# Optimization experiments

Hardware: AMD Instinct MI355X
Metric: run time of the kernel (lower is better)

Reference implementation:

```python
import jax, jax.numpy as jnp
import numpy as np


def _attention(q, k, v, causal):
    # q,k,v: (B, S, H, D) -> matches flash_attn_func input layout
    B, Sq, H, D = q.shape
    Sk = k.shape[1]
    scale = 1.0 / jnp.sqrt(jnp.asarray(D, dtype=q.dtype))
    # scores: (B, H, Sq, Sk)
    scores = jnp.einsum('bqhd,bkhd->bhqk', q, k) * scale
    if causal:
        # position i attends to j <= i (standard causal mask, Sq == Sk here)
        mask = jnp.tril(jnp.ones((Sq, Sk), dtype=bool))
        scores = jnp.where(mask[None, None], scores, jnp.asarray(-jnp.inf, dtype=scores.dtype))
    probs = jax.nn.softmax(scores, axis=-1)
    out = jnp.einsum('bhqk,bkhd->bqhd', probs, v)
    return out


def setup_inputs() -> dict:
    key = jax.random.key(0)
    kq, kk, kv = jax.random.split(key, 3)
    B, S, H, D = 2, 2048, 16, 128
    q = jax.random.normal(kq, (B, S, H, D), dtype=jnp.float32)
    k = jax.random.normal(kk, (B, S, H, D), dtype=jnp.float32)
    v = jax.random.normal(kv, (B, S, H, D), dtype=jnp.float32)
    return {"q": q, "k": k, "v": v, "causal": 1}


def reference(q, k, v, causal):
    return _attention(q, k, v, bool(causal))
```

## Files before the change

kernel.cpp:

```cpp
#include <hip/hip_runtime.h>

typedef short bf16x8 __attribute__((ext_vector_type(8)));
typedef float f32x16 __attribute__((ext_vector_type(16)));

constexpr int S = 2048;
constexpr int H = 16;
constexpr int D = 128;
constexpr int BM = 128;
constexpr int TILE = 8192;
constexpr int KSTR = 136;
constexpr int MST  = 33;


__device__ inline unsigned int pk2(float a, float b) {
    unsigned int ua = __builtin_bit_cast(unsigned int, a);
    unsigned int ub = __builtin_bit_cast(unsigned int, b);
    ua += 0x7fffu + ((ua >> 16) & 1u);
    ub += 0x7fffu + ((ub >> 16) & 1u);
    return (ua >> 16) | (ub & 0xffff0000u);
}

__global__ __launch_bounds__(256) void cvt_kv(const float* __restrict__ K,
                                              const float* __restrict__ V,
                                              unsigned short* __restrict__ Kb,
                                              unsigned short* __restrict__ Vtb) {
    __shared__ unsigned short Kst[64 * KSTR];
    __shared__ unsigned short Vst[64 * KSTR];
    __shared__ unsigned short Vout[TILE];
    const int tid = threadIdx.x;
    const int t   = blockIdx.x;
    const int bh  = blockIdx.y;
    const int b = bh >> 4, h = bh & 15;
    const size_t base = ((size_t)(b * S + t * 64) * H + h) * D;

    #pragma unroll
    for (int u = 0; u < 4; ++u) {
        const int c   = tid + 256 * u;
        const int n   = c >> 4;
        const int off = (c & 15) * 8;
        const float* pk = K + base + (size_t)n * (H * D) + off;
        float4 f0 = *(const float4*)pk;
        float4 f1 = *(const float4*)(pk + 4);
        unsigned int w[4];
        w[0] = pk2(f0.x, f0.y); w[1] = pk2(f0.z, f0.w);
        w[2] = pk2(f1.x, f1.y); w[3] = pk2(f1.z, f1.w);
        *(uint4*)&Kst[n * KSTR + off] = *(const uint4*)w;
        const float* pv = V + base + (size_t)n * (H * D) + off;
        f0 = *(const float4*)pv;
        f1 = *(const float4*)(pv + 4);
        w[0] = pk2(f0.x, f0.y); w[1] = pk2(f0.z, f0.w);
        w[2] = pk2(f1.x, f1.y); w[3] = pk2(f1.z, f1.w);
        *(uint4*)&Vst[n * KSTR + off] = *(const uint4*)w;
    }
    __syncthreads();

    unsigned short* outK = Kb + ((size_t)bh * 32 + t) * TILE;
    #pragma unroll
    for (int u = 0; u < 4; ++u) {
        const int s = u * 256 + tid;
        const int chunk = s >> 6;
        const int row   = s & 63;
        *(uint4*)(outK + s * 8) = *(const uint4*)&Kst[row * KSTR + chunk * 8];
    }

    const int d  = tid >> 1;
    const int kh = (tid & 1) * 32;
    unsigned short tmp[32];
    #pragma unroll
    for (int m = 0; m < 32; ++m) {
        const int sig = kh + m;
        const int k = (sig & ~12) | ((sig & 4) << 1) | ((sig & 8) >> 1);
        tmp[m] = Vst[k * KSTR + d];
    }
    #pragma unroll
    for (int uu = 0; uu < 4; ++uu) {
        const int cc = (kh >> 3) + uu;
        *(uint4*)&Vout[(cc * 128 + d) * 8] = *(const uint4*)&tmp[uu * 8];
    }
    __syncthreads();
    unsigned short* outV = Vtb + ((size_t)bh * 32 + t) * TILE;
    #pragma unroll
    for (int u = 0; u < 4; ++u) {
        const int s = u * 256 + tid;
        *(uint4*)(outV + s * 8) = *(const uint4*)&Vout[s * 8];
    }
}

__global__ __launch_bounds__(512, 2) void fa_fwd(
    const float* __restrict__ Q,
    const unsigned short* __restrict__ Kb,
    const unsigned short* __restrict__ Vtb,
    const int* __restrict__ causal_p,
    float* __restrict__ Op)
{
    __shared__ float mbf[4][64 * MST];
    __shared__ float lbf[4][32];

    const int tid  = threadIdx.x;
    const int w    = tid >> 6;
    const int lane = tid & 63;
    const int ln   = lane & 31;
    const int half = lane >> 5;
    const int qw   = w & 3;
    const int nt   = w >> 2;

    int bh, qp;
    if (gridDim.x == 8 && gridDim.y == 32) {
        const int lid = blockIdx.x + (blockIdx.y << 3);
        const int xcd = lid & 7;
        const int ii  = lid >> 3;
        bh = (xcd << 2) + (ii & 3);
        qp = ii >> 2;
    } else {
        bh = blockIdx.y;
        qp = blockIdx.x;
    }
    const int b = bh >> 4;
    const int h = bh & 15;
    const int causal = *causal_p;
    const float cfold = 0.12751743f;

    const unsigned short* Kc = Kb  + (size_t)bh * (32 * TILE);
    const unsigned short* Vc = Vtb + (size_t)bh * (32 * TILE);
    const int koff  = half * 512 + nt * 256 + ln * 8;
    const int vkoff = (nt * 4 + half) * 1024 + ln * 8;

    #pragma unroll 1
    for (int ph = 0; ph < 2; ++ph) {
        const int qblk  = ph ? (15 - qp) : qp;
        const int q0    = qblk * BM;
        const int qrow0 = q0 + qw * 32;
        const int jmax  = causal ? ((q0 + BM - 1) >> 6) : (S / 64 - 1);

        bf16x8 qf[8];
        {
            const size_t rowoff = ((size_t)(b * S + qrow0 + ln) * H + h) * D;
            #pragma unroll
            for (int c = 0; c < 8; ++c) {
                float4 f0 = *(const float4*)(Q + rowoff + c * 16 + half * 8);
                float4 f1 = *(const float4*)(Q + rowoff + c * 16 + half * 8 + 4);
                unsigned int t[4];
                t[0] = pk2(f0.x * cfold, f0.y * cfold);
                t[1] = pk2(f0.z * cfold, f0.w * cfold);
                t[2] = pk2(f1.x * cfold, f1.y * cfold);
                t[3] = pk2(f1.z * cfold, f1.w * cfold);
                qf[c] = *(const bf16x8*)t;
            }
        }

        f32x16 o[4];
        #pragma unroll
        for (int dt = 0; dt < 4; ++dt)
            #pragma unroll
            for (int r = 0; r < 16; ++r) o[dt][r] = 0.0f;
        float l0 = 0.0f, l1 = 0.0f;

        uint4 kr[8], vr[8];
        if ((!causal) || (nt * 32 <= qrow0 + 31)) {
            #pragma unroll
            for (int c = 0; c < 8; ++c)
                kr[c] = *(const uint4*)(Kc + c * 1024 + koff);
            #pragma unroll
            for (int i = 0; i < 8; ++i)
                vr[i] = *(const uint4*)(Vc + (i >> 2) * 2048 + (i & 3) * 256 + vkoff);
        }

        #pragma unroll 1
        for (int j = 0; j <= jmax; ++j) {
            const bool aj = (!causal) || (j * 64 + nt * 32 <= qrow0 + 31);
            const bool an = (j < jmax) &&
                            ((!causal) || ((j + 1) * 64 + nt * 32 <= qrow0 + 31));

            f32x16 sacc;
            if (aj) {
                #pragma unroll
                for (int r = 0; r < 16; ++r) sacc[r] = 0.0f;
                __builtin_amdgcn_s_setprio(1);
                #pragma unroll
                for (int c = 0; c < 8; ++c) {
                    bf16x8 kf = *(const bf16x8*)&kr[c];
                    sacc = __builtin_amdgcn_mfma_f32_32x32x16_bf16(kf, qf[c], sacc, 0, 0, 0);
                }
                __builtin_amdgcn_s_setprio(0);
            }
            if (an) {
                const unsigned short* kt = Kc + (size_t)(j + 1) * TILE;
                #pragma unroll
                for (int c = 0; c < 8; ++c)
                    kr[c] = *(const uint4*)(kt + c * 1024 + koff);
            }

            if (aj) {
                const int thr  = qrow0 + ln - j * 64;
                const bool full = (!causal) || (j * 64 + 63 <= qrow0);
                __builtin_amdgcn_s_setprio(1);
                #pragma unroll
                for (int win2 = 0; win2 < 2; ++win2) {
                    unsigned int pw[4];
                    #pragma unroll
                    for (int d2 = 0; d2 < 4; ++d2) {
                        const int r0 = win2 * 8 + 2 * d2;
                        const int r1 = r0 + 1;
                        float e0 = __builtin_amdgcn_exp2f(sacc[r0]);
                        float e1 = __builtin_amdgcn_exp2f(sacc[r1]);
                        if (!full) {
                            const int k0 = nt * 32 + (r0 & 3) + 8 * (r0 >> 2) + 4 * half;
                            const int k1 = nt * 32 + (r1 & 3) + 8 * (r1 >> 2) + 4 * half;
                            if (k0 > thr) e0 = 0.0f;
                            if (k1 > thr) e1 = 0.0f;
                        }
                        l0 += e0; l1 += e1;
                        pw[d2] = pk2(e0, e1);
                    }
                    bf16x8 pf = *(const bf16x8*)pw;
                    #pragma unroll
                    for (int dt = 0; dt < 4; ++dt) {
                        bf16x8 vf = *(const bf16x8*)&vr[win2 * 4 + dt];
                        o[dt] = __builtin_amdgcn_mfma_f32_32x32x16_bf16(vf, pf, o[dt], 0, 0, 0);
                    }
                }
                __builtin_amdgcn_s_setprio(0);
            }
            if (an) {
                const unsigned short* vt = Vc + (size_t)(j + 1) * TILE;
                #pragma unroll
                for (int i = 0; i < 8; ++i)
                    vr[i] = *(const uint4*)(vt + (i >> 2) * 2048 + (i & 3) * 256 + vkoff);
            }
        }

        const float l = l0 + l1;
        const float lp = l + __shfl_xor(l, 32);
        float* mb = mbf[qw];
        if (w >= 4) {
            #pragma unroll
            for (int dt = 0; dt < 2; ++dt)
                #pragma unroll
                for (int r = 0; r < 16; ++r)
                    mb[lane * MST + dt * 16 + r] = o[dt][r];
            if (half == 0) lbf[qw][ln] = lp;
        }
        __syncthreads();
        float ltot = 1.0f;
        if (w < 4) {
            #pragma unroll
            for (int dt = 0; dt < 2; ++dt)
                #pragma unroll
                for (int r = 0; r < 16; ++r)
                    o[dt][r] += mb[lane * MST + dt * 16 + r];
            ltot = lp + lbf[qw][ln];
        }
        __syncthreads();
        if (w >= 4) {
            #pragma unroll
            for (int dt = 2; dt < 4; ++dt)
                #pragma unroll
                for (int r = 0; r < 16; ++r)
                    mb[lane * MST + (dt - 2) * 16 + r] = o[dt][r];
        }
        __syncthreads();
        if (w < 4) {
            #pragma unroll
            for (int dt = 2; dt < 4; ++dt)
                #pragma unroll
                for (int r = 0; r < 16; ++r)
                    o[dt][r] += mb[lane * MST + (dt - 2) * 16 + r];

            const float inv = 1.0f / ltot;
            float* op = Op + ((size_t)(b * S + qrow0 + ln) * H + h) * D;
            #pragma unroll
            for (int dt = 0; dt < 4; ++dt)
                #pragma unroll
                for (int rq = 0; rq < 4; ++rq) {
                    float4 st;
                    st.x = o[dt][rq * 4 + 0] * inv;
                    st.y = o[dt][rq * 4 + 1] * inv;
                    st.z = o[dt][rq * 4 + 2] * inv;
                    st.w = o[dt][rq * 4 + 3] * inv;
                    *(float4*)(op + dt * 32 + 8 * rq + 4 * half) = st;
                }
        }
        __syncthreads();
    }
}

extern "C" void kernel_launch(void* const* d_in, const int* in_sizes, int n_in,
                              void* d_out, int out_size, void* d_ws, size_t ws_size,
                              hipStream_t stream) {
    const int B = in_sizes[0] / (S * H * D);
    unsigned short* Kb  = (unsigned short*)d_ws;
    unsigned short* Vtb = Kb + (size_t)B * S * H * D;

    cvt_kv<<<dim3(S / 64, B * H), 256, 0, stream>>>(
        (const float*)d_in[1], (const float*)d_in[2], Kb, Vtb);
    fa_fwd<<<dim3(8, B * H), 512, 0, stream>>>(
        (const float*)d_in[0], Kb, Vtb, (const int*)d_in[3], (float*)d_out);
}
```

Baseline: 187.2 us.

## Split KV tiles across two wave groups with 1024-thread blocks

Doubles the block to 16 waves, so each query block's KV tiles are split between two wave groups that take alternating 64-key tiles. The partial O and row sums from the three extra groups are merged through enlarged shared buffers before the final normalisation. This shortens each wave's serial KV loop and raises the waves in flight per block. In exchange it allows only one block per CU, uses more shared memory, and adds a heavier reduction step.

New measurement: 738.4 us. 295% more time.

```diff
diff --git a/kernel.cpp b/kernel.cpp
--- a/kernel.cpp
+++ b/kernel.cpp
@@ -86,15 +86,15 @@
     }
 }
 
-__global__ __launch_bounds__(512, 2) void fa_fwd(
+__global__ __launch_bounds__(1024, 1) void fa_fwd(
     const float* __restrict__ Q,
     const unsigned short* __restrict__ Kb,
     const unsigned short* __restrict__ Vtb,
     const int* __restrict__ causal_p,
     float* __restrict__ Op)
 {
-    __shared__ float mbf[4][64 * MST];
-    __shared__ float lbf[4][32];
+    __shared__ float mbf[3][4][64 * MST];
+    __shared__ float lbf[3][4][32];
 
     const int tid  = threadIdx.x;
     const int w    = tid >> 6;
@@ -102,7 +102,9 @@
     const int ln   = lane & 31;
     const int half = lane >> 5;
     const int qw   = w & 3;
-    const int nt   = w >> 2;
+    const int nt   = (w >> 2) & 1;
+    const int jt   = w >> 3;
+    const int pi   = w >> 2;
 
     int bh, qp;
     if (gridDim.x == 8 && gridDim.y == 32) {
@@ -130,7 +132,8 @@
         const int qblk  = ph ? (15 - qp) : qp;
         const int q0    = qblk * BM;
         const int qrow0 = q0 + qw * 32;
-        const int jmax  = causal ? ((q0 + BM - 1) >> 6) : (S / 64 - 1);
+        const int T     = causal ? (2 * qblk + 2) : (S / 64);
+        const int I     = T >> 1;
 
         bf16x8 qf[8];
         {
@@ -156,20 +159,23 @@
         float l0 = 0.0f, l1 = 0.0f;
 
         uint4 kr[8], vr[8];
-        if ((!causal) || (nt * 32 <= qrow0 + 31)) {
+        if ((!causal) || (jt * 64 + nt * 32 <= qrow0 + 31)) {
+            const unsigned short* kt = Kc + (size_t)jt * TILE;
+            const unsigned short* vt = Vc + (size_t)jt * TILE;
             #pragma unroll
             for (int c = 0; c < 8; ++c)
-                kr[c] = *(const uint4*)(Kc + c * 1024 + koff);
+                kr[c] = *(const uint4*)(kt + c * 1024 + koff);
             #pragma unroll
             for (int i = 0; i < 8; ++i)
-                vr[i] = *(const uint4*)(Vc + (i >> 2) * 2048 + (i & 3) * 256 + vkoff);
+                vr[i] = *(const uint4*)(vt + (i >> 2) * 2048 + (i & 3) * 256 + vkoff);
         }
 
         #pragma unroll 1
-        for (int j = 0; j <= jmax; ++j) {
-            const bool aj = (!causal) || (j * 64 + nt * 32 <= qrow0 + 31);
-            const bool an = (j < jmax) &&
-                            ((!causal) || ((j + 1) * 64 + nt * 32 <= qrow0 + 31));
+        for (int i = 0; i < I; ++i) {
+            const int jj = 2 * i + jt;
+            const bool aj = (!causal) || (jj * 64 + nt * 32 <= qrow0 + 31);
+            const bool an = (i + 1 < I) &&
+                            ((!causal) || ((jj + 2) * 64 + nt * 32 <= qrow0 + 31));
 
             f32x16 sacc;
             if (aj) {
@@ -184,15 +190,15 @@
                 __builtin_amdgcn_s_setprio(0);
             }
             if (an) {
-                const unsigned short* kt = Kc + (size_t)(j + 1) * TILE;
+                const unsigned short* kt = Kc + (size_t)(jj + 2) * TILE;
                 #pragma unroll
                 for (int c = 0; c < 8; ++c)
                     kr[c] = *(const uint4*)(kt + c * 1024 + koff);
             }
 
             if (aj) {
-                const int thr  = qrow0 + ln - j * 64;
-                const bool full = (!causal) || (j * 64 + 63 <= qrow0);
+                const int thr  = qrow0 + ln - jj * 64;
+                const bool full = (!causal) || (jj * 64 + 63 <= qrow0);
                 __builtin_amdgcn_s_setprio(1);
                 #pragma unroll
                 for (int win2 = 0; win2 < 2; ++win2) {
@@ -222,36 +228,42 @@
                 __builtin_amdgcn_s_setprio(0);
             }
             if (an) {
-                const unsigned short* vt = Vc + (size_t)(j + 1) * TILE;
-                #pragma unroll
-                for (int i = 0; i < 8; ++i)
-                    vr[i] = *(const uint4*)(vt + (i >> 2) * 2048 + (i & 3) * 256 + vkoff);
+                const unsigned short* vt = Vc + (size_t)(jj + 2) * TILE;
+                #pragma unroll
+                for (int i2 = 0; i2 < 8; ++i2)
+                    vr[i2] = *(const uint4*)(vt + (i2 >> 2) * 2048 + (i2 & 3) * 256 + vkoff);
             }
         }
 
         const float l = l0 + l1;
         const float lp = l + __shfl_xor(l, 32);
-        float* mb = mbf[qw];
-        if (w >= 4) {
+        float ltot = 1.0f;
+        if (pi > 0) {
+            float* mb = &mbf[pi - 1][qw][0];
             #pragma unroll
             for (int dt = 0; dt < 2; ++dt)
                 #pragma unroll
                 for (int r = 0; r < 16; ++r)
                     mb[lane * MST + dt * 16 + r] = o[dt][r];
-            if (half == 0) lbf[qw][ln] = lp;
+            if (half == 0) lbf[pi - 1][qw][ln] = lp;
         }
         __syncthreads();
-        float ltot = 1.0f;
-        if (w < 4) {
-            #pragma unroll
-            for (int dt = 0; dt < 2; ++dt)
-                #pragma unroll
-                for (int r = 0; r < 16; ++r)
-                    o[dt][r] += mb[lane * MST + dt * 16 + r];
-            ltot = lp + lbf[qw][ln];
+        if (pi == 0) {
+            ltot = lp;
+            #pragma unroll
+            for (int s = 0; s < 3; ++s) {
+                const float* mb = &mbf[s][qw][0];
+                #pragma unroll
+                for (int dt = 0; dt < 2; ++dt)
+                    #pragma unroll
+                    for (int r = 0; r < 16; ++r)
+                        o[dt][r] += mb[lane * MST + dt * 16 + r];
+                ltot += lbf[s][qw][ln];
+            }
         }
         __syncthreads();
-        if (w >= 4) {
+        if (pi > 0) {
+            float* mb = &mbf[pi - 1][qw][0];
             #pragma unroll
             for (int dt = 2; dt < 4; ++dt)
                 #pragma unroll
@@ -259,12 +271,16 @@
                     mb[lane * MST + (dt - 2) * 16 + r] = o[dt][r];
         }
         __syncthreads();
-        if (w < 4) {
-            #pragma unroll
-            for (int dt = 2; dt < 4; ++dt)
-                #pragma unroll
-                for (int r = 0; r < 16; ++r)
-                    o[dt][r] += mb[lane * MST + (dt - 2) * 16 + r];
+        if (pi == 0) {
+            #pragma unroll
+            for (int s = 0; s < 3; ++s) {
+                const float* mb = &mbf[s][qw][0];
+                #pragma unroll
+                for (int dt = 2; dt < 4; ++dt)
+                    #pragma unroll
+                    for (int r = 0; r < 16; ++r)
+                        o[dt][r] += mb[lane * MST + (dt - 2) * 16 + r];
+            }
 
             const float inv = 1.0f / ltot;
             float* op = Op + ((size_t)(b * S + qrow0 + ln) * H + h) * D;
@@ -293,6 +309,6 @@
 
     cvt_kv<<<dim3(S / 64, B * H), 256, 0, stream>>>(
         (const float*)d_in[1], (const float*)d_in[2], Kb, Vtb);
-    fa_fwd<<<dim3(8, B * H), 512, 0, stream>>>(
+    fa_fwd<<<dim3(8, B * H), 1024, 0, stream>>>(
         (const float*)d_in[0], Kb, Vtb, (const int*)d_in[3], (float*)d_out);
 }
```

## Split head dimension across blocks and drop register prefetch for higher occupancy

Applied to the files above, without the earlier changes.

Doubles the grid by assigning each block half of the output head dimension, so each wave keeps only two PV accumulators. The next-tile K/V register prefetch is removed in favor of loading inside the loop, and the occupancy hint is raised to four waves per EU. The aim is more concurrent waves to hide latency and fewer registers. In exchange, the QK^T product and the K loads are duplicated across the two head-dimension halves.

New measurement: 276.1 us. 1.48x slower.

```diff
diff --git a/kernel.cpp b/kernel.cpp
--- a/kernel.cpp
+++ b/kernel.cpp
@@ -86,7 +86,9 @@
     }
 }
 
-__global__ __launch_bounds__(512, 2) void fa_fwd(
+__global__ __launch_bounds__(512)
+__attribute__((amdgpu_waves_per_eu(4)))
+void fa_fwd(
     const float* __restrict__ Q,
     const unsigned short* __restrict__ Kb,
     const unsigned short* __restrict__ Vtb,
@@ -104,16 +106,19 @@
     const int qw   = w & 3;
     const int nt   = w >> 2;
 
-    int bh, qp;
-    if (gridDim.x == 8 && gridDim.y == 32) {
-        const int lid = blockIdx.x + (blockIdx.y << 3);
+    int bh, qp, dh;
+    if (gridDim.x == 16 && gridDim.y == 32) {
+        const int lid = blockIdx.x + (blockIdx.y << 4);
         const int xcd = lid & 7;
         const int ii  = lid >> 3;
         bh = (xcd << 2) + (ii & 3);
-        qp = ii >> 2;
+        const int rest = ii >> 2;
+        qp = rest & 7;
+        dh = rest >> 3;
     } else {
         bh = blockIdx.y;
-        qp = blockIdx.x;
+        qp = blockIdx.x & 7;
+        dh = blockIdx.x >> 3;
     }
     const int b = bh >> 4;
     const int h = bh & 15;
@@ -148,136 +153,106 @@
             }
         }
 
-        f32x16 o[4];
+        f32x16 o[2];
         #pragma unroll
-        for (int dt = 0; dt < 4; ++dt)
-            #pragma unroll
-            for (int r = 0; r < 16; ++r) o[dt][r] = 0.0f;
+        for (int dt2 = 0; dt2 < 2; ++dt2)
+            #pragma unroll
+            for (int r = 0; r < 16; ++r) o[dt2][r] = 0.0f;
         float l0 = 0.0f, l1 = 0.0f;
-
-        uint4 kr[8], vr[8];
-        if ((!causal) || (nt * 32 <= qrow0 + 31)) {
-            #pragma unroll
-            for (int c = 0; c < 8; ++c)
-                kr[c] = *(const uint4*)(Kc + c * 1024 + koff);
-            #pragma unroll
-            for (int i = 0; i < 8; ++i)
-                vr[i] = *(const uint4*)(Vc + (i >> 2) * 2048 + (i & 3) * 256 + vkoff);
-        }
 
         #pragma unroll 1
         for (int j = 0; j <= jmax; ++j) {
             const bool aj = (!causal) || (j * 64 + nt * 32 <= qrow0 + 31);
-            const bool an = (j < jmax) &&
-                            ((!causal) || ((j + 1) * 64 + nt * 32 <= qrow0 + 31));
+            if (!aj) continue;
+
+            const unsigned short* kt = Kc + (size_t)j * TILE;
+            const unsigned short* vt = Vc + (size_t)j * TILE;
+
+            uint4 kr[8];
+            #pragma unroll
+            for (int c = 0; c < 8; ++c)
+                kr[c] = *(const uint4*)(kt + c * 1024 + koff);
+            uint4 vr[4];
+            #pragma unroll
+            for (int i = 0; i < 4; ++i)
+                vr[i] = *(const uint4*)(vt + vkoff + (i >> 1) * 2048 +
+                                        (dh * 2 + (i & 1)) * 256);
 
             f32x16 sacc;
-            if (aj) {
-                #pragma unroll
-                for (int r = 0; r < 16; ++r) sacc[r] = 0.0f;
-                __builtin_amdgcn_s_setprio(1);
-                #pragma unroll
-                for (int c = 0; c < 8; ++c) {
-                    bf16x8 kf = *(const bf16x8*)&kr[c];
-                    sacc = __builtin_amdgcn_mfma_f32_32x32x16_bf16(kf, qf[c], sacc, 0, 0, 0);
+            #pragma unroll
+            for (int r = 0; r < 16; ++r) sacc[r] = 0.0f;
+            __builtin_amdgcn_s_setprio(1);
+            #pragma unroll
+            for (int c = 0; c < 8; ++c) {
+                bf16x8 kf = *(const bf16x8*)&kr[c];
+                sacc = __builtin_amdgcn_mfma_f32_32x32x16_bf16(kf, qf[c], sacc, 0, 0, 0);
+            }
+            __builtin_amdgcn_s_setprio(0);
+
+            const int thr  = qrow0 + ln - j * 64;
+            const bool full = (!causal) || (j * 64 + 63 <= qrow0);
+            __builtin_amdgcn_s_setprio(1);
+            #pragma unroll
+            for (int win2 = 0; win2 < 2; ++win2) {
+                unsigned int pw[4];
+                #pragma unroll
+                for (int d2 = 0; d2 < 4; ++d2) {
+                    const int r0 = win2 * 8 + 2 * d2;
+                    const int r1 = r0 + 1;
+                    float e0 = __builtin_amdgcn_exp2f(sacc[r0]);
+                    float e1 = __builtin_amdgcn_exp2f(sacc[r1]);
+                    if (!full) {
+                        const int k0 = nt * 32 + (r0 & 3) + 8 * (r0 >> 2) + 4 * half;
+                        const int k1 = nt * 32 + (r1 & 3) + 8 * (r1 >> 2) + 4 * half;
+                        if (k0 > thr) e0 = 0.0f;
+                        if (k1 > thr) e1 = 0.0f;
+                    }
+                    l0 += e0; l1 += e1;
+                    pw[d2] = pk2(e0, e1);
                 }
-                __builtin_amdgcn_s_setprio(0);
+                bf16x8 pf = *(const bf16x8*)pw;
+                #pragma unroll
+                for (int dt2 = 0; dt2 < 2; ++dt2) {
+                    bf16x8 vf = *(const bf16x8*)&vr[win2 * 2 + dt2];
+                    o[dt2] = __builtin_amdgcn_mfma_f32_32x32x16_bf16(vf, pf, o[dt2], 0, 0, 0);
+                }
             }
-            if (an) {
-                const unsigned short* kt = Kc + (size_t)(j + 1) * TILE;
-                #pragma unroll
-                for (int c = 0; c < 8; ++c)
-                    kr[c] = *(const uint4*)(kt + c * 1024 + koff);
-            }
-
-            if (aj) {
-                const int thr  = qrow0 + ln - j * 64;
-                const bool full = (!causal) || (j * 64 + 63 <= qrow0);
-                __builtin_amdgcn_s_setprio(1);
-                #pragma unroll
-                for (int win2 = 0; win2 < 2; ++win2) {
-                    unsigned int pw[4];
-                    #pragma unroll
-                    for (int d2 = 0; d2 < 4; ++d2) {
-                        const int r0 = win2 * 8 + 2 * d2;
-                        const int r1 = r0 + 1;
-                        float e0 = __builtin_amdgcn_exp2f(sacc[r0]);
-                        float e1 = __builtin_amdgcn_exp2f(sacc[r1]);
-                        if (!full) {
-                            const int k0 = nt * 32 + (r0 & 3) + 8 * (r0 >> 2) + 4 * half;
-                            const int k1 = nt * 32 + (r1 & 3) + 8 * (r1 >> 2) + 4 * half;
-                            if (k0 > thr) e0 = 0.0f;
-                            if (k1 > thr) e1 = 0.0f;
-                        }
-                        l0 += e0; l1 += e1;
-                        pw[d2] = pk2(e0, e1);
-                    }
-                    bf16x8 pf = *(const bf16x8*)pw;
-                    #pragma unroll
-                    for (int dt = 0; dt < 4; ++dt) {
-                        bf16x8 vf = *(const bf16x8*)&vr[win2 * 4 + dt];
-                        o[dt] = __builtin_amdgcn_mfma_f32_32x32x16_bf16(vf, pf, o[dt], 0, 0, 0);
-                    }
-                }
-                __builtin_amdgcn_s_setprio(0);
-            }
-            if (an) {
-                const unsigned short* vt = Vc + (size_t)(j + 1) * TILE;
-                #pragma unroll
-                for (int i = 0; i < 8; ++i)
-                    vr[i] = *(const uint4*)(vt + (i >> 2) * 2048 + (i & 3) * 256 + vkoff);
-            }
+            __builtin_amdgcn_s_setprio(0);
         }
 
         const float l = l0 + l1;
         const float lp = l + __shfl_xor(l, 32);
-        float* mb = mbf[qw];
-        if (w >= 4) {
-            #pragma unroll
-            for (int dt = 0; dt < 2; ++dt)
+        if (nt == 1) {
+            float* mb = mbf[qw];
+            #pragma unroll
+            for (int dt2 = 0; dt2 < 2; ++dt2)
                 #pragma unroll
                 for (int r = 0; r < 16; ++r)
-                    mb[lane * MST + dt * 16 + r] = o[dt][r];
+                    mb[lane * MST + dt2 * 16 + r] = o[dt2][r];
             if (half == 0) lbf[qw][ln] = lp;
         }
         __syncthreads();
-        float ltot = 1.0f;
-        if (w < 4) {
-            #pragma unroll
-            for (int dt = 0; dt < 2; ++dt)
+        if (nt == 0) {
+            const float* mb = mbf[qw];
+            #pragma unroll
+            for (int dt2 = 0; dt2 < 2; ++dt2)
                 #pragma unroll
                 for (int r = 0; r < 16; ++r)
-                    o[dt][r] += mb[lane * MST + dt * 16 + r];
-            ltot = lp + lbf[qw][ln];
-        }
-        __syncthreads();
-        if (w >= 4) {
-            #pragma unroll
-            for (int dt = 2; dt < 4; ++dt)
-                #pragma unroll
-                for (int r = 0; r < 16; ++r)
-                    mb[lane * MST + (dt - 2) * 16 + r] = o[dt][r];
-        }
-        __syncthreads();
-        if (w < 4) {
-            #pragma unroll
-            for (int dt = 2; dt < 4; ++dt)
-                #pragma unroll
-                for (int r = 0; r < 16; ++r)
-                    o[dt][r] += mb[lane * MST + (dt - 2) * 16 + r];
+                    o[dt2][r] += mb[lane * MST + dt2 * 16 + r];
+            const float ltot = lp + lbf[qw][ln];
 
             const float inv = 1.0f / ltot;
             float* op = Op + ((size_t)(b * S + qrow0 + ln) * H + h) * D;
             #pragma unroll
-            for (int dt = 0; dt < 4; ++dt)
+            for (int dt2 = 0; dt2 < 2; ++dt2)
                 #pragma unroll
                 for (int rq = 0; rq < 4; ++rq) {
                     float4 st;
-                    st.x = o[dt][rq * 4 + 0] * inv;
-                    st.y = o[dt][rq * 4 + 1] * inv;
-                    st.z = o[dt][rq * 4 + 2] * inv;
-                    st.w = o[dt][rq * 4 + 3] * inv;
-                    *(float4*)(op + dt * 32 + 8 * rq + 4 * half) = st;
+                    st.x = o[dt2][rq * 4 + 0] * inv;
+                    st.y = o[dt2][rq * 4 + 1] * inv;
+                    st.z = o[dt2][rq * 4 + 2] * inv;
+                    st.w = o[dt2][rq * 4 + 3] * inv;
+                    *(float4*)(op + (dh * 2 + dt2) * 32 + 8 * rq + 4 * half) = st;
                 }
         }
         __syncthreads();
@@ -293,6 +268,6 @@
 
     cvt_kv<<<dim3(S / 64, B * H), 256, 0, stream>>>(
         (const float*)d_in[1], (const float*)d_in[2], Kb, Vtb);
-    fa_fwd<<<dim3(8, B * H), 512, 0, stream>>>(
+    fa_fwd<<<dim3(16, B * H), 512, 0, stream>>>(
         (const float*)d_in[0], Kb, Vtb, (const int*)d_in[3], (float*)d_out);
 }
```
